# Kernel optimization log

Hardware: AMD Instinct MI355X
Metric: run time of the kernel (lower is better)

The kernel has to match this reference:

```python
import jax, jax.numpy as jnp
import numpy as np

B, T, V, H, C = 512, 512, 64, 128, 4


def setup_inputs() -> dict:
    key = jax.random.key(0)
    ks = jax.random.split(key, 32)
    s = 0.05  # weight scale
    inp = {
        'x': jax.random.normal(ks[0], (B, T, V), jnp.float32),
        'd': jax.random.uniform(ks[1], (B, T, 1), jnp.float32),
        'm1': (jax.random.uniform(ks[2], (B, T, V)) < 0.5).astype(jnp.float32),
        'h0_1': 0.1 * jax.random.normal(ks[3], (B, H), jnp.float32),
        'h0_2': 0.1 * jax.random.normal(ks[4], (B, H), jnp.float32),
        'h0_3': 0.1 * jax.random.normal(ks[5], (B, H), jnp.float32),
        'W_ih1': s * jax.random.normal(ks[6], (3 * H, V), jnp.float32),
        'W_hh1': s * jax.random.normal(ks[7], (3 * H, H), jnp.float32),
        'b_ih1': jnp.zeros((3 * H,), jnp.float32),
        'b_hh1': jnp.zeros((3 * H,), jnp.float32),
        'W_ih2': s * jax.random.normal(ks[8], (3 * H, H), jnp.float32),
        'W_hh2': s * jax.random.normal(ks[9], (3 * H, H), jnp.float32),
        'b_ih2': jnp.zeros((3 * H,), jnp.float32),
        'b_hh2': jnp.zeros((3 * H,), jnp.float32),
        'W_ih3': s * jax.random.normal(ks[10], (3 * H, H), jnp.float32),
        'W_hh3': s * jax.random.normal(ks[11], (3 * H, H), jnp.float32),
        'b_ih3': jnp.zeros((3 * H,), jnp.float32),
        'b_hh3': jnp.zeros((3 * H,), jnp.float32),
        'W_out': s * jax.random.normal(ks[12], (C, H), jnp.float32),
        'b_out': jax.random.uniform(ks[13], (C,), jnp.float32),
        'W_dx': s * jax.random.normal(ks[14], (V, 1), jnp.float32),
        'b_dx': jax.random.uniform(ks[15], (V,), jnp.float32),
        'W_dh': s * jax.random.normal(ks[16], (H, 1), jnp.float32),
        'b_dh': jax.random.uniform(ks[17], (H,), jnp.float32),
    }
    return inp


def _gru_cell(xt, h, Wih, Whh, bih, bhh):
    # torch.nn.GRUCell math
    gi = xt @ Wih.T + bih          # [B, 3H]
    gh = h @ Whh.T + bhh           # [B, 3H]
    ir, iz, inn = jnp.split(gi, 3, axis=1)
    hr, hz, hn = jnp.split(gh, 3, axis=1)
    r = jax.nn.sigmoid(ir + hr)
    z = jax.nn.sigmoid(iz + hz)
    n = jnp.tanh(inn + r * hn)
    return (1.0 - z) * n + z * h


def reference(x, d, m1, h0_1, h0_2, h0_3,
              W_ih1, W_hh1, b_ih1, b_hh1,
              W_ih2, W_hh2, b_ih2, b_hh2,
              W_ih3, W_hh3, b_ih3, b_hh3,
              W_out, b_out, W_dx, b_dx, W_dh, b_dh):
    x0 = x[:, 0, :]  # first observation used for imputation

    def head(h):
        return jax.nn.softmax(h @ W_out.T + b_out, axis=1)

    # t = 0: no decay, raw input
    h1 = _gru_cell(x0, h0_1, W_ih1, W_hh1, b_ih1, b_hh1)
    h2 = _gru_cell(h1, h0_2, W_ih2, W_hh2, b_ih2, b_hh2)
    h3 = _gru_cell(h2, h0_3, W_ih3, W_hh3, b_ih3, b_hh3)
    y0 = head(h3)

    # time-major scan inputs for t = 1..T-1
    xs = (jnp.swapaxes(x[:, 1:, :], 0, 1),   # x_t
          jnp.swapaxes(x[:, :-1, :], 0, 1),  # x_{t-1}
          jnp.swapaxes(m1[:, 1:, :], 0, 1),  # m_t
          jnp.swapaxes(d[:, 1:, :], 0, 1))   # d_t [T-1, B, 1]

    def step(carry, inp):
        h1, h2, h3 = carry
        xt, xp, mt, dt = inp
        gamma_h = jnp.exp(-jax.nn.relu(dt @ W_dh.T + b_dh))  # [B, H]
        h1 = h1 * gamma_h
        h2 = h2 * gamma_h
        h3 = h3 * gamma_h
        gamma_x = jnp.exp(-jax.nn.relu(dt @ W_dx.T + b_dx))  # [B, V]
        x1 = (xp * gamma_x + (1.0 - gamma_x) * x0) * (1.0 - mt) + mt * xt
        h1 = _gru_cell(x1, h1, W_ih1, W_hh1, b_ih1, b_hh1)
        h2 = _gru_cell(h1, h2, W_ih2, W_hh2, b_ih2, b_hh2)
        h3 = _gru_cell(h2, h3, W_ih3, W_hh3, b_ih3, b_hh3)
        return (h1, h2, h3), head(h3)

    _, ys = jax.lax.scan(step, (h1, h2, h3), xs)  # [T-1, B, C]
    Y = jnp.concatenate([y0[None], ys], axis=0)    # [T, B, C]
    return jnp.swapaxes(Y, 0, 1)                   # [B, T, C]
```

## Files before the change

### kernel.cpp

```cpp
#include <hip/hip_runtime.h>

#define TT 512
#define VV 64
#define RING 16

typedef _Float16 f16;
typedef f16 f16x8 __attribute__((ext_vector_type(8)));
typedef f16 f16x4 __attribute__((ext_vector_type(4)));
typedef float f32x4v __attribute__((ext_vector_type(4)));
typedef unsigned long long u64;
typedef unsigned u32;

typedef __attribute__((address_space(1))) unsigned gu32;
typedef __attribute__((address_space(1))) unsigned long long gu64;

#define MFMA(A_,B_,C_) __builtin_amdgcn_mfma_f32_16x16x32_f16((A_),(B_),(C_),0,0,0)
#define AT_LD32(p)   __hip_atomic_load((gu32*)(void*)(p), __ATOMIC_RELAXED, __HIP_MEMORY_SCOPE_AGENT)
#define AT_ST32(p,v) __hip_atomic_store((gu32*)(void*)(p),(v), __ATOMIC_RELAXED, __HIP_MEMORY_SCOPE_AGENT)
#define AT_LD64(p)   __hip_atomic_load((gu64*)(void*)(p), __ATOMIC_RELAXED, __HIP_MEMORY_SCOPE_AGENT)
#define AT_ST64(p,v) __hip_atomic_store((gu64*)(void*)(p),(v), __ATOMIC_RELAXED, __HIP_MEMORY_SCOPE_AGENT)

__device__ __forceinline__ void barrier_lds(){ asm volatile("s_waitcnt lgkmcnt(0)\n\ts_barrier" ::: "memory"); }
__device__ __forceinline__ void wait_vm0(){ asm volatile("s_waitcnt vmcnt(0)" ::: "memory"); }
__device__ __forceinline__ float4 ld4(const float* p){ return *(const float4*)p; }

__device__ __forceinline__ f16x8 ldA8(const float* p){
  f16x8 a;
  #pragma unroll
  for (int j = 0; j < 8; ++j) a[j] = (f16)p[j];
  return a;
}

__device__ __forceinline__ int fragOff16(int d0, int b){
  const int kt = d0 >> 5, qq = (d0 >> 3) & 3, j0 = d0 & 7;
  return (kt*64 + qq*16 + b)*8 + j0;
}

__device__ __forceinline__ void fragW_lds(f16x8* buf, int d0, int b, const float* h4){
  f16x4 v;
  #pragma unroll
  for (int e = 0; e < 4; ++e) v[e] = (f16)h4[e];
  *(f16x4*)((f16*)buf + fragOff16(d0, b)) = v;
}

__device__ __forceinline__ void pubFrag(char* slot, int d0, int b, const float* h4){
  union { f16x4 v; u64 u; } uu;
  #pragma unroll
  for (int e = 0; e < 4; ++e) uu.v[e] = (f16)h4[e];
  AT_ST64((u64*)(slot + fragOff16(d0, b)*2), uu.u);
}

__device__ __forceinline__ f16x8 impFrag(const char* slot, int kt, int lane){
  union { u64 u[2]; f16x8 v; } vv;
  const u64* p = (const u64*)(slot + (kt*64 + lane)*16);
  vv.u[0] = AT_LD64((u64*)p);
  vv.u[1] = AT_LD64((u64*)(p + 1));
  return vv.v;
}

__device__ __forceinline__ void spin_ge(u32* f, u32 val){
  if ((threadIdx.x & 63) == 0){
    u32 g = 0;
    while (AT_LD32(f) < val && ++g < (1u << 20)) {}
  }
  asm volatile("" ::: "memory");
}

__device__ __forceinline__ void gates_upd(const f32x4v* Ci, const f32x4v* Ch,
                                          const float* bR, const float* bZ,
                                          const float* bI, const float* bH,
                                          float* hp){
  #pragma unroll
  for (int e = 0; e < 4; ++e){
    float rr = 1.f/(1.f + __expf(-(Ci[0][e] + Ch[0][e] + bR[e])));
    float zz = 1.f/(1.f + __expf(-(Ci[1][e] + Ch[1][e] + bZ[e])));
    float nv = Ci[2][e] + bI[e] + rr*(Ch[2][e] + bH[e]);
    float nn = 1.f - 2.f/(1.f + __expf(2.f*nv));
    hp[e] = (1.f - zz)*nn + zz*hp[e];
  }
}

__global__ void k_init(u32* wsf){
  const int i = blockIdx.x*256 + threadIdx.x;
  if (i < 4096) AT_ST32(wsf + i, 0u);
}

__launch_bounds__(512, 1)
__global__ void k_pipe(const float* __restrict__ x,   const float* __restrict__ dd,
                       const float* __restrict__ m1,
                       const float* __restrict__ h01, const float* __restrict__ h02,
                       const float* __restrict__ h03,
                       const float* __restrict__ Wih1, const float* __restrict__ Whh1,
                       const float* __restrict__ bih1, const float* __restrict__ bhh1,
                       const float* __restrict__ Wih2, const float* __restrict__ Whh2,
                       const float* __restrict__ bih2, const float* __restrict__ bhh2,
                       const float* __restrict__ Wih3, const float* __restrict__ Whh3,
                       const float* __restrict__ bih3, const float* __restrict__ bhh3,
                       const float* __restrict__ Wout, const float* __restrict__ bout,
                       const float* __restrict__ Wdx,  const float* __restrict__ bdx,
                       const float* __restrict__ Wdh,  const float* __restrict__ bdh,
                       float* __restrict__ y, u32* __restrict__ wsf, char* __restrict__ wsd)
{
  __shared__ f16x8 sFrag[2][256];
  __shared__ f16x8 sX1[2][128];
  __shared__ f16x8 sHead[2][256];

  const int tid = threadIdx.x, wid = tid >> 6, lane = tid & 63;
  const int q = lane >> 4, r = lane & 15;
  const int blk = blockIdx.x, role = blk >> 5, grp = blk & 31, b0 = grp << 4;

  u32* const FL  = wsf;
  u32* const ACK = wsf + 1024;
  u32* const fl0 = FL  + grp*16;
  u32* const ak0 = ACK + grp*16;
  u32* const fl1 = FL  + (32+grp)*16;
  u32* const ak1 = ACK + (32+grp)*16;
  char* const ring0 = wsd + (size_t)grp*RING*4096;
  char* const ring1 = wsd + (size_t)(32+grp)*RING*4096;

  const int dG = wid*16 + 4*q;

  const float* bihX = (role == 0) ? bih1 : (role == 1) ? bih2 : bih3;
  const float* bhhX = (role == 0) ? bhh1 : (role == 1) ? bhh2 : bhh3;
  const float* h0X  = (role == 0) ? h01  : (role == 1) ? h02  : h03;

  float bR[4], bZ[4], bI[4], bH[4], hS[4], WdhL[4], bdhL[4];
  #pragma unroll
  for (int e = 0; e < 4; ++e){
    const int d = dG + e;
    bR[e] = bihX[d] + bhhX[d];
    bZ[e] = bihX[128+d] + bhhX[128+d];
    bI[e] = bihX[256+d];
    bH[e] = bhhX[256+d];
    WdhL[e] = Wdh[d]; bdhL[e] = bdh[d];
  }
  { float4 a = ld4(h0X + (size_t)(b0+r)*128 + dG); hS[0]=a.x; hS[1]=a.y; hS[2]=a.z; hS[3]=a.w; }
  float dhC = 0.f, dhN = dd[(size_t)(b0+r)*TT + 1];

  if (role == 0){
    f16x8 Ai[3][2], Ah[3][4];
    #pragma unroll
    for (int g = 0; g < 3; ++g){
      const int mrow = (g*8 + wid)*16 + r;
      #pragma unroll
      for (int kt = 0; kt < 2; ++kt) Ai[g][kt] = ldA8(Wih1 + mrow*64 + kt*32 + q*8);
      #pragma unroll
      for (int kt = 0; kt < 4; ++kt) Ah[g][kt] = ldA8(Whh1 + mrow*128 + kt*32 + q*8);
    }
    const int bx = (wid & 3)*4 + q, v0 = 4*r;
    float Wdx4[4] = {0,0,0,0}, bdx4[4] = {0,0,0,0};
    float4 xC = {0,0,0,0}, x0v = {0,0,0,0}, xN = {0,0,0,0}, mN = {0,0,0,0};
    float4 xP = {0,0,0,0}, mC = {0,0,0,0};
    float dxC = 0.f, dxN = 0.f;
    if (wid < 4){
      #pragma unroll
      for (int e = 0; e < 4; ++e){ Wdx4[e] = Wdx[v0+e]; bdx4[e] = bdx[v0+e]; }
      xC  = ld4(x + ((size_t)(b0+bx)*TT + 0)*VV + v0);
      x0v = xC;
      xN  = ld4(x  + ((size_t)(b0+bx)*TT + 1)*VV + v0);
      mN  = ld4(m1 + ((size_t)(b0+bx)*TT + 1)*VV + v0);
      dxN = dd[(size_t)(b0+bx)*TT + 1];
      xP = xC; mC = mN; dxC = dxN;
    }
    __syncthreads();

    for (int t = 0; t < TT; ++t){
      const int par = t & 1;
      if ((t & 3) == 0 && t >= 16) spin_ge(ak0, (u32)(t-13));
      if (wid < 4){
        float xi[4];
        if (t == 0){ xi[0]=xC.x; xi[1]=xC.y; xi[2]=xC.z; xi[3]=xC.w; }
        else {
          const float* xc = (const float*)&xC; const float* xp = (const float*)&xP;
          const float* x0e = (const float*)&x0v; const float* me = (const float*)&mC;
          #pragma unroll
          for (int e = 0; e < 4; ++e){
            float gx = __expf(-fmaxf(dxC*Wdx4[e] + bdx4[e], 0.f));
            xi[e] = (xp[e]*gx + (1.f-gx)*x0e[e])*(1.f-me[e]) + me[e]*xc[e];
          }
        }
        fragW_lds(&sX1[par][0], v0, bx, xi);
      }
      if (t >= 1){
        #pragma unroll
        for (int e = 0; e < 4; ++e)
          hS[e] *= __expf(-fmaxf(dhC*WdhL[e] + bdhL[e], 0.f));
      }
      fragW_lds(&sFrag[par][0], dG, r, hS);
      barrier_lds();
      f16x8 bx1[2], bh4[4];
      #pragma unroll
      for (int kt = 0; kt < 2; ++kt) bx1[kt] = sX1[par][kt*64 + lane];
      #pragma unroll
      for (int kt = 0; kt < 4; ++kt) bh4[kt] = sFrag[par][kt*64 + lane];
      f32x4v Ci[3], Ch[3];
      #pragma unroll
      for (int g = 0; g < 3; ++g){ Ci[g] = (f32x4v){0,0,0,0}; Ch[g] = (f32x4v){0,0,0,0}; }
      #pragma unroll
      for (int g = 0; g < 3; ++g){
        #pragma unroll
        for (int kt = 0; kt < 4; ++kt) Ch[g] = MFMA(Ah[g][kt], bh4[kt], Ch[g]);
        #pragma unroll
        for (int kt = 0; kt < 2; ++kt) Ci[g] = MFMA(Ai[g][kt], bx1[kt], Ci[g]);
      }
      gates_upd(Ci, Ch, bR, bZ, bI, bH, hS);
      pubFrag(ring0 + (size_t)(t & (RING-1))*4096, dG, r, hS);
      if ((t & 3) == 3){
        wait_vm0();
        barrier_lds();
        if (tid == 0) AT_ST32(fl0, (u32)(t+1));
      }
      dhC = dhN;
      const int tp = (t+2 < TT) ? (t+2) : (TT-1);
      dhN = dd[(size_t)(b0+r)*TT + tp];
      if (wid < 4){
        xP = xC; xC = xN; mC = mN; dxC = dxN;
        xN  = ld4(x  + ((size_t)(b0+bx)*TT + tp)*VV + v0);
        mN  = ld4(m1 + ((size_t)(b0+bx)*TT + tp)*VV + v0);
        dxN = dd[(size_t)(b0+bx)*TT + tp];
      }
    }
    return;
  }

  if (role == 1){
    f16x8 Ai[3][4], Ah[3][4];
    #pragma unroll
    for (int g = 0; g < 3; ++g){
      const int mrow = (g*8 + wid)*16 + r;
      #pragma unroll
      for (int kt = 0; kt < 4; ++kt){
        Ai[g][kt] = ldA8(Wih2 + mrow*128 + kt*32 + q*8);
        Ah[g][kt] = ldA8(Whh2 + mrow*128 + kt*32 + q*8);
      }
    }
    __syncthreads();

    spin_ge(fl0, 8u);
    f16x8 bi[4], biN[4];
    #pragma unroll
    for (int kt = 0; kt < 4; ++kt) bi[kt] = impFrag(ring0, kt, lane);

    for (int t = 0; t < TT; ++t){
      const int par = t & 1;
      if ((t & 3) == 0 && t >= 16) spin_ge(ak1, (u32)(t-13));
      if (t + 1 < TT){
        const char* sIn = ring0 + (size_t)((t+1) & (RING-1))*4096;
        #pragma unroll
        for (int kt = 0; kt < 4; ++kt) biN[kt] = impFrag(sIn, kt, lane);
      }
      if (t >= 1){
        #pragma unroll
        for (int e = 0; e < 4; ++e)
          hS[e] *= __expf(-fmaxf(dhC*WdhL[e] + bdhL[e], 0.f));
      }
      fragW_lds(&sFrag[par][0], dG, r, hS);
      barrier_lds();
      if (tid == 0) AT_ST32(ak0, (u32)t);
      f16x8 bh4[4];
      #pragma unroll
      for (int kt = 0; kt < 4; ++kt) bh4[kt] = sFrag[par][kt*64 + lane];
      f32x4v Ci[3], Ch[3];
      #pragma unroll
      for (int g = 0; g < 3; ++g){ Ci[g] = (f32x4v){0,0,0,0}; Ch[g] = (f32x4v){0,0,0,0}; }
      #pragma unroll
      for (int g = 0; g < 3; ++g){
        #pragma unroll
        for (int kt = 0; kt < 4; ++kt) Ch[g] = MFMA(Ah[g][kt], bh4[kt], Ch[g]);
        #pragma unroll
        for (int kt = 0; kt < 4; ++kt) Ci[g] = MFMA(Ai[g][kt], bi[kt], Ci[g]);
      }
      gates_upd(Ci, Ch, bR, bZ, bI, bH, hS);
      pubFrag(ring1 + (size_t)(t & (RING-1))*4096, dG, r, hS);
      if ((t & 3) == 3){
        wait_vm0();
        barrier_lds();
        if (tid == 0) AT_ST32(fl1, (u32)(t+1));
        if (t < TT-1) spin_ge(fl0, (u32)(t+7 <= TT ? t+7 : TT));
      }
      if (t + 1 < TT){
        #pragma unroll
        for (int kt = 0; kt < 4; ++kt) bi[kt] = biN[kt];
      }
      dhC = dhN;
      const int tp = (t+2 < TT) ? (t+2) : (TT-1);
      dhN = dd[(size_t)(b0+r)*TT + tp];
    }
    return;
  }

  {
    f16x8 Ai[3][4], Ah[3][4];
    #pragma unroll
    for (int g = 0; g < 3; ++g){
      const int mrow = (g*8 + wid)*16 + r;
      #pragma unroll
      for (int kt = 0; kt < 4; ++kt){
        Ai[g][kt] = ldA8(Wih3 + mrow*128 + kt*32 + q*8);
        Ah[g][kt] = ldA8(Whh3 + mrow*128 + kt*32 + q*8);
      }
    }
    f16x8 aO[4]; float bo4[4] = {0,0,0,0};
    if (wid == 4){
      #pragma unroll
      for (int kt = 0; kt < 4; ++kt){
        f16x8 a;
        #pragma unroll
        for (int j = 0; j < 8; ++j)
          a[j] = (r < 4) ? (f16)Wout[r*128 + kt*32 + q*8 + j] : (f16)0.f;
        aO[kt] = a;
      }
      #pragma unroll
      for (int e = 0; e < 4; ++e) bo4[e] = bout[e];
    }
    __syncthreads();

    spin_ge(fl1, 8u);
    f16x8 bi[4], biN[4];
    #pragma unroll
    for (int kt = 0; kt < 4; ++kt) bi[kt] = impFrag(ring1, kt, lane);

    for (int s = 0; s <= TT; ++s){
      const int par = s & 1;
      fragW_lds(&sHead[par][0], dG, r, hS);
      if (s < TT){
        if (s + 1 < TT){
          const char* sIn = ring1 + (size_t)((s+1) & (RING-1))*4096;
          #pragma unroll
          for (int kt = 0; kt < 4; ++kt) biN[kt] = impFrag(sIn, kt, lane);
        }
        if (s >= 1){
          #pragma unroll
          for (int e = 0; e < 4; ++e)
            hS[e] *= __expf(-fmaxf(dhC*WdhL[e] + bdhL[e], 0.f));
        }
        fragW_lds(&sFrag[par][0], dG, r, hS);
      }
      barrier_lds();
      if (s < TT && tid == 0) AT_ST32(ak1, (u32)s);
      if (s < TT){
        f16x8 bh4[4];
        #pragma unroll
        for (int kt = 0; kt < 4; ++kt) bh4[kt] = sFrag[par][kt*64 + lane];
        f32x4v Ci[3], Ch[3];
        #pragma unroll
        for (int g = 0; g < 3; ++g){ Ci[g] = (f32x4v){0,0,0,0}; Ch[g] = (f32x4v){0,0,0,0}; }
        #pragma unroll
        for (int g = 0; g < 3; ++g){
          #pragma unroll
          for (int kt = 0; kt < 4; ++kt) Ch[g] = MFMA(Ah[g][kt], bh4[kt], Ch[g]);
          #pragma unroll
          for (int kt = 0; kt < 4; ++kt) Ci[g] = MFMA(Ai[g][kt], bi[kt], Ci[g]);
        }
        gates_upd(Ci, Ch, bR, bZ, bI, bH, hS);
      }
      if (s >= 1 && wid == 4){
        f32x4v cl = {0.f,0.f,0.f,0.f};
        #pragma unroll
        for (int kt = 0; kt < 4; ++kt) cl = MFMA(aO[kt], sHead[par][kt*64 + lane], cl);
        if (lane < 16){
          float l0 = cl[0]+bo4[0], l1 = cl[1]+bo4[1], l2 = cl[2]+bo4[2], l3 = cl[3]+bo4[3];
          float mx = fmaxf(fmaxf(l0,l1), fmaxf(l2,l3));
          float e0 = __expf(l0-mx), e1 = __expf(l1-mx), e2 = __expf(l2-mx), e3 = __expf(l3-mx);
          float inv = 1.f/(e0+e1+e2+e3);
          float4 o; o.x = e0*inv; o.y = e1*inv; o.z = e2*inv; o.w = e3*inv;
          *(float4*)(y + ((size_t)(b0+lane)*TT + (s-1))*4) = o;
        }
      }
      if ((s & 3) == 3 && s < TT-1) spin_ge(fl1, (u32)(s+7 <= TT ? s+7 : TT));
      if (s + 1 < TT){
        #pragma unroll
        for (int kt = 0; kt < 4; ++kt) bi[kt] = biN[kt];
      }
      dhC = dhN;
      const int tp = (s+2 < TT) ? (s+2) : (TT-1);
      dhN = dd[(size_t)(b0+r)*TT + tp];
    }
  }
}

extern "C" void kernel_launch(void* const* d_in, const int* in_sizes, int n_in,
                              void* d_out, int out_size, void* d_ws, size_t ws_size,
                              hipStream_t stream) {
  (void)in_sizes; (void)n_in; (void)out_size; (void)ws_size;
  u32*  wsf = (u32*)d_ws;
  char* wsd = (char*)d_ws + 16384;
  k_init<<<dim3(16), dim3(256), 0, stream>>>(wsf);
  k_pipe<<<dim3(96), dim3(512), 0, stream>>>(
      (const float*)d_in[0],  (const float*)d_in[1],  (const float*)d_in[2],
      (const float*)d_in[3],  (const float*)d_in[4],  (const float*)d_in[5],
      (const float*)d_in[6],  (const float*)d_in[7],  (const float*)d_in[8],  (const float*)d_in[9],
      (const float*)d_in[10], (const float*)d_in[11], (const float*)d_in[12], (const float*)d_in[13],
      (const float*)d_in[14], (const float*)d_in[15], (const float*)d_in[16], (const float*)d_in[17],
      (const float*)d_in[18], (const float*)d_in[19],
      (const float*)d_in[20], (const float*)d_in[21],
      (const float*)d_in[22], (const float*)d_in[23],
      (float*)d_out, wsf, wsd);
}
```

Measured before the change: 1.282 ms.

## Move one weight matrix per stage to LDS and fuse r/z accumulators

Each pipeline stage now keeps one of its two GRU weight matrices in shared memory (96 KB of fragments) instead of registers. The r and z gate accumulators are merged into single MFMA chains over both input and hidden products. The next-step input fragments are loaded after the MFMAs into the same registers, dropping the double buffer. This cuts VGPR pressure and possible spills, at the cost of extra LDS reads every step inside the serial recurrence and a later prefetch issue point.

Measured after the change: 1.266 ms. About the same (-1.3%).

```diff
diff --git a/kernel.cpp b/kernel.cpp
--- a/kernel.cpp
+++ b/kernel.cpp
@@ -66,15 +66,16 @@
   asm volatile("" ::: "memory");
 }
 
-__device__ __forceinline__ void gates_upd(const f32x4v* Ci, const f32x4v* Ch,
-                                          const float* bR, const float* bZ,
-                                          const float* bI, const float* bH,
-                                          float* hp){
+__device__ __forceinline__ void gates_upd2(const f32x4v& C0, const f32x4v& C1,
+                                           const f32x4v& Ci2, const f32x4v& Ch2,
+                                           const float* bR, const float* bZ,
+                                           const float* bI, const float* bH,
+                                           float* hp){
   #pragma unroll
   for (int e = 0; e < 4; ++e){
-    float rr = 1.f/(1.f + __expf(-(Ci[0][e] + Ch[0][e] + bR[e])));
-    float zz = 1.f/(1.f + __expf(-(Ci[1][e] + Ch[1][e] + bZ[e])));
-    float nv = Ci[2][e] + bI[e] + rr*(Ch[2][e] + bH[e]);
+    float rr = 1.f/(1.f + __expf(-(C0[e] + bR[e])));
+    float zz = 1.f/(1.f + __expf(-(C1[e] + bZ[e])));
+    float nv = Ci2[e] + bI[e] + rr*(Ch2[e] + bH[e]);
     float nn = 1.f - 2.f/(1.f + __expf(2.f*nv));
     hp[e] = (1.f - zz)*nn + zz*hp[e];
   }
@@ -101,6 +102,7 @@
                        const float* __restrict__ Wdh,  const float* __restrict__ bdh,
                        float* __restrict__ y, u32* __restrict__ wsf, char* __restrict__ wsd)
 {
+  __shared__ f16x8 sW[8*12*64];
   __shared__ f16x8 sFrag[2][256];
   __shared__ f16x8 sX1[2][128];
   __shared__ f16x8 sHead[2][256];
@@ -119,6 +121,7 @@
   char* const ring1 = wsd + (size_t)(32+grp)*RING*4096;
 
   const int dG = wid*16 + 4*q;
+  const int wbase = wid*12;
 
   const float* bihX = (role == 0) ? bih1 : (role == 1) ? bih2 : bih3;
   const float* bhhX = (role == 0) ? bhh1 : (role == 1) ? bhh2 : bhh3;
@@ -138,14 +141,15 @@
   float dhC = 0.f, dhN = dd[(size_t)(b0+r)*TT + 1];
 
   if (role == 0){
-    f16x8 Ai[3][2], Ah[3][4];
+    f16x8 Ai[3][2];
     #pragma unroll
     for (int g = 0; g < 3; ++g){
       const int mrow = (g*8 + wid)*16 + r;
       #pragma unroll
       for (int kt = 0; kt < 2; ++kt) Ai[g][kt] = ldA8(Wih1 + mrow*64 + kt*32 + q*8);
       #pragma unroll
-      for (int kt = 0; kt < 4; ++kt) Ah[g][kt] = ldA8(Whh1 + mrow*128 + kt*32 + q*8);
+      for (int kt = 0; kt < 4; ++kt)
+        sW[(wbase + g*4 + kt)*64 + lane] = ldA8(Whh1 + mrow*128 + kt*32 + q*8);
     }
     const int bx = (wid & 3)*4 + q, v0 = 4*r;
     float Wdx4[4] = {0,0,0,0}, bdx4[4] = {0,0,0,0};
@@ -193,17 +197,20 @@
       for (int kt = 0; kt < 2; ++kt) bx1[kt] = sX1[par][kt*64 + lane];
       #pragma unroll
       for (int kt = 0; kt < 4; ++kt) bh4[kt] = sFrag[par][kt*64 + lane];
-      f32x4v Ci[3], Ch[3];
-      #pragma unroll
-      for (int g = 0; g < 3; ++g){ Ci[g] = (f32x4v){0,0,0,0}; Ch[g] = (f32x4v){0,0,0,0}; }
-      #pragma unroll
-      for (int g = 0; g < 3; ++g){
-        #pragma unroll
-        for (int kt = 0; kt < 4; ++kt) Ch[g] = MFMA(Ah[g][kt], bh4[kt], Ch[g]);
-        #pragma unroll
-        for (int kt = 0; kt < 2; ++kt) Ci[g] = MFMA(Ai[g][kt], bx1[kt], Ci[g]);
-      }
-      gates_upd(Ci, Ch, bR, bZ, bI, bH, hS);
+      f32x4v C0 = {0,0,0,0}, C1 = {0,0,0,0}, Ci2 = {0,0,0,0}, Ch2 = {0,0,0,0};
+      #pragma unroll
+      for (int kt = 0; kt < 4; ++kt) C0  = MFMA(sW[(wbase + 0*4 + kt)*64 + lane], bh4[kt], C0);
+      #pragma unroll
+      for (int kt = 0; kt < 4; ++kt) C1  = MFMA(sW[(wbase + 1*4 + kt)*64 + lane], bh4[kt], C1);
+      #pragma unroll
+      for (int kt = 0; kt < 4; ++kt) Ch2 = MFMA(sW[(wbase + 2*4 + kt)*64 + lane], bh4[kt], Ch2);
+      #pragma unroll
+      for (int kt = 0; kt < 2; ++kt) C0  = MFMA(Ai[0][kt], bx1[kt], C0);
+      #pragma unroll
+      for (int kt = 0; kt < 2; ++kt) C1  = MFMA(Ai[1][kt], bx1[kt], C1);
+      #pragma unroll
+      for (int kt = 0; kt < 2; ++kt) Ci2 = MFMA(Ai[2][kt], bx1[kt], Ci2);
+      gates_upd2(C0, C1, Ci2, Ch2, bR, bZ, bI, bH, hS);
       pubFrag(ring0 + (size_t)(t & (RING-1))*4096, dG, r, hS);
       if ((t & 3) == 3){
         wait_vm0();
@@ -224,31 +231,26 @@
   }
 
   if (role == 1){
-    f16x8 Ai[3][4], Ah[3][4];
+    f16x8 Ah[3][4];
     #pragma unroll
     for (int g = 0; g < 3; ++g){
       const int mrow = (g*8 + wid)*16 + r;
       #pragma unroll
       for (int kt = 0; kt < 4; ++kt){
-        Ai[g][kt] = ldA8(Wih2 + mrow*128 + kt*32 + q*8);
+        sW[(wbase + g*4 + kt)*64 + lane] = ldA8(Wih2 + mrow*128 + kt*32 + q*8);
         Ah[g][kt] = ldA8(Whh2 + mrow*128 + kt*32 + q*8);
       }
     }
     __syncthreads();
 
     spin_ge(fl0, 8u);
-    f16x8 bi[4], biN[4];
+    f16x8 bi[4];
     #pragma unroll
     for (int kt = 0; kt < 4; ++kt) bi[kt] = impFrag(ring0, kt, lane);
 
     for (int t = 0; t < TT; ++t){
       const int par = t & 1;
       if ((t & 3) == 0 && t >= 16) spin_ge(ak1, (u32)(t-13));
-      if (t + 1 < TT){
-        const char* sIn = ring0 + (size_t)((t+1) & (RING-1))*4096;
-        #pragma unroll
-        for (int kt = 0; kt < 4; ++kt) biN[kt] = impFrag(sIn, kt, lane);
-      }
       if (t >= 1){
         #pragma unroll
         for (int e = 0; e < 4; ++e)
@@ -260,17 +262,25 @@
       f16x8 bh4[4];
       #pragma unroll
       for (int kt = 0; kt < 4; ++kt) bh4[kt] = sFrag[par][kt*64 + lane];
-      f32x4v Ci[3], Ch[3];
-      #pragma unroll
-      for (int g = 0; g < 3; ++g){ Ci[g] = (f32x4v){0,0,0,0}; Ch[g] = (f32x4v){0,0,0,0}; }
-      #pragma unroll
-      for (int g = 0; g < 3; ++g){
-        #pragma unroll
-        for (int kt = 0; kt < 4; ++kt) Ch[g] = MFMA(Ah[g][kt], bh4[kt], Ch[g]);
-        #pragma unroll
-        for (int kt = 0; kt < 4; ++kt) Ci[g] = MFMA(Ai[g][kt], bi[kt], Ci[g]);
-      }
-      gates_upd(Ci, Ch, bR, bZ, bI, bH, hS);
+      f32x4v C0 = {0,0,0,0}, C1 = {0,0,0,0}, Ci2 = {0,0,0,0}, Ch2 = {0,0,0,0};
+      #pragma unroll
+      for (int kt = 0; kt < 4; ++kt) C0  = MFMA(Ah[0][kt], bh4[kt], C0);
+      #pragma unroll
+      for (int kt = 0; kt < 4; ++kt) C1  = MFMA(Ah[1][kt], bh4[kt], C1);
+      #pragma unroll
+      for (int kt = 0; kt < 4; ++kt) Ch2 = MFMA(Ah[2][kt], bh4[kt], Ch2);
+      #pragma unroll
+      for (int kt = 0; kt < 4; ++kt) C0  = MFMA(sW[(wbase + 0*4 + kt)*64 + lane], bi[kt], C0);
+      #pragma unroll
+      for (int kt = 0; kt < 4; ++kt) C1  = MFMA(sW[(wbase + 1*4 + kt)*64 + lane], bi[kt], C1);
+      #pragma unroll
+      for (int kt = 0; kt < 4; ++kt) Ci2 = MFMA(sW[(wbase + 2*4 + kt)*64 + lane], bi[kt], Ci2);
+      if (t + 1 < TT){
+        const char* sIn = ring0 + (size_t)((t+1) & (RING-1))*4096;
+        #pragma unroll
+        for (int kt = 0; kt < 4; ++kt) bi[kt] = impFrag(sIn, kt, lane);
+      }
+      gates_upd2(C0, C1, Ci2, Ch2, bR, bZ, bI, bH, hS);
       pubFrag(ring1 + (size_t)(t & (RING-1))*4096, dG, r, hS);
       if ((t & 3) == 3){
         wait_vm0();
@@ -278,10 +288,6 @@
         if (tid == 0) AT_ST32(fl1, (u32)(t+1));
         if (t < TT-1) spin_ge(fl0, (u32)(t+7 <= TT ? t+7 : TT));
       }
-      if (t + 1 < TT){
-        #pragma unroll
-        for (int kt = 0; kt < 4; ++kt) bi[kt] = biN[kt];
-      }
       dhC = dhN;
       const int tp = (t+2 < TT) ? (t+2) : (TT-1);
       dhN = dd[(size_t)(b0+r)*TT + tp];
@@ -290,13 +296,13 @@
   }
 
   {
-    f16x8 Ai[3][4], Ah[3][4];
+    f16x8 Ah[3][4];
     #pragma unroll
     for (int g = 0; g < 3; ++g){
       const int mrow = (g*8 + wid)*16 + r;
       #pragma unroll
       for (int kt = 0; kt < 4; ++kt){
-        Ai[g][kt] = ldA8(Wih3 + mrow*128 + kt*32 + q*8);
+        sW[(wbase + g*4 + kt)*64 + lane] = ldA8(Wih3 + mrow*128 + kt*32 + q*8);
         Ah[g][kt] = ldA8(Whh3 + mrow*128 + kt*32 + q*8);
       }
     }
@@ -316,7 +322,7 @@
     __syncthreads();
 
     spin_ge(fl1, 8u);
-    f16x8 bi[4], biN[4];
+    f16x8 bi[4];
     #pragma unroll
     for (int kt = 0; kt < 4; ++kt) bi[kt] = impFrag(ring1, kt, lane);
 
@@ -324,11 +330,6 @@
       const int par = s & 1;
       fragW_lds(&sHead[par][0], dG, r, hS);
       if (s < TT){
-        if (s + 1 < TT){
-          const char* sIn = ring1 + (size_t)((s+1) & (RING-1))*4096;
-          #pragma unroll
-          for (int kt = 0; kt < 4; ++kt) biN[kt] = impFrag(sIn, kt, lane);
-        }
         if (s >= 1){
           #pragma unroll
           for (int e = 0; e < 4; ++e)
@@ -342,17 +343,25 @@
         f16x8 bh4[4];
         #pragma unroll
         for (int kt = 0; kt < 4; ++kt) bh4[kt] = sFrag[par][kt*64 + lane];
-        f32x4v Ci[3], Ch[3];
-        #pragma unroll
-        for (int g = 0; g < 3; ++g){ Ci[g] = (f32x4v){0,0,0,0}; Ch[g] = (f32x4v){0,0,0,0}; }
-        #pragma unroll
-        for (int g = 0; g < 3; ++g){
+        f32x4v C0 = {0,0,0,0}, C1 = {0,0,0,0}, Ci2 = {0,0,0,0}, Ch2 = {0,0,0,0};
+        #pragma unroll
+        for (int kt = 0; kt < 4; ++kt) C0  = MFMA(Ah[0][kt], bh4[kt], C0);
+        #pragma unroll
+        for (int kt = 0; kt < 4; ++kt) C1  = MFMA(Ah[1][kt], bh4[kt], C1);
+        #pragma unroll
+        for (int kt = 0; kt < 4; ++kt) Ch2 = MFMA(Ah[2][kt], bh4[kt], Ch2);
+        #pragma unroll
+        for (int kt = 0; kt < 4; ++kt) C0  = MFMA(sW[(wbase + 0*4 + kt)*64 + lane], bi[kt], C0);
+        #pragma unroll
+        for (int kt = 0; kt < 4; ++kt) C1  = MFMA(sW[(wbase + 1*4 + kt)*64 + lane], bi[kt], C1);
+        #pragma unroll
+        for (int kt = 0; kt < 4; ++kt) Ci2 = MFMA(sW[(wbase + 2*4 + kt)*64 + lane], bi[kt], Ci2);
+        if (s + 1 < TT){
+          const char* sIn = ring1 + (size_t)((s+1) & (RING-1))*4096;
           #pragma unroll
-          for (int kt = 0; kt < 4; ++kt) Ch[g] = MFMA(Ah[g][kt], bh4[kt], Ch[g]);
-          #pragma unroll
-          for (int kt = 0; kt < 4; ++kt) Ci[g] = MFMA(Ai[g][kt], bi[kt], Ci[g]);
+          for (int kt = 0; kt < 4; ++kt) bi[kt] = impFrag(sIn, kt, lane);
         }
-        gates_upd(Ci, Ch, bR, bZ, bI, bH, hS);
+        gates_upd2(C0, C1, Ci2, Ch2, bR, bZ, bI, bH, hS);
       }
       if (s >= 1 && wid == 4){
         f32x4v cl = {0.f,0.f,0.f,0.f};
@@ -368,10 +377,6 @@
         }
       }
       if ((s & 3) == 3 && s < TT-1) spin_ge(fl1, (u32)(s+7 <= TT ? s+7 : TT));
-      if (s + 1 < TT){
-        #pragma unroll
-        for (int kt = 0; kt < 4; ++kt) bi[kt] = biN[kt];
-      }
       dhC = dhN;
       const int tp = (s+2 < TT) ? (s+2) : (TT-1);
       dhN = dd[(size_t)(b0+r)*TT + tp];
```
